# Kernel tuning notes

Measured on AMD Instinct MI355X. Metric: run time of the kernel, lower is better.

Reference implementation:

```python
import jax, jax.numpy as jnp
import numpy as np

N, K, D, H = 16384, 8, 128, 256  # nodes, preds per node, emb dim, hidden


def _build_graph():
    i = np.arange(1, N + 1)[:, None]      # [N,1] node ids 1..N
    k = np.arange(K)[None, :]             # [1,K]
    pred = i - 1 - k                       # predecessor node ids
    mask = pred >= 0
    pred_nodes = np.maximum(pred, 0).astype(np.int32)        # [N,K]
    end = np.repeat(np.arange(1, N + 1), K).astype(np.int32)  # [N*K]
    edges = np.stack([pred_nodes.reshape(-1), end], axis=1)   # [E,2]
    pred_edge_idx = (np.arange(N * K).reshape(N, K) + 1).astype(np.int32)  # +1: zero row prepended to distances
    return pred_nodes, pred_edge_idx, mask, edges.astype(np.int32)


def setup_inputs() -> dict:
    key = jax.random.key(0)
    k1, k2, k3 = jax.random.split(key, 3)
    pred_nodes, pred_edge_idx, mask, edges = _build_graph()
    s1 = 1.0 / np.sqrt(2 * D)
    s2 = 1.0 / np.sqrt(H)
    return {
        "words_embs": jax.random.normal(k1, (N + 1, D), dtype=jnp.float32),
        "W1": jax.random.uniform(k2, (2 * D, H), jnp.float32, -s1, s1),
        "b1": jnp.zeros((H,), jnp.float32),
        "W2": jax.random.uniform(k3, (H, 1), jnp.float32, -s2, s2),
        "b2": jnp.zeros((1,), jnp.float32),
        "best_idxs": jnp.arange(N + 1, dtype=jnp.int32),  # the chain path 0->1->...->N
        "edges": jnp.asarray(edges),
        "pred_nodes": jnp.asarray(pred_nodes),
        "pred_edge_idx": jnp.asarray(pred_edge_idx),
        "pred_mask": jnp.asarray(mask),
    }


def _distance(x, y, W1, b1, W2, b2):
    # MLP over concatenated pair features: Linear -> Tanh -> Linear -> Softplus
    h = jnp.tanh(jnp.concatenate([x, y], axis=-1) @ W1 + b1)
    return jax.nn.softplus(h @ W2 + b2)  # [...,1]


def _forward_alg(words_embs, edges, pred_nodes, pred_edge_idx, pred_mask, W1, b1, W2, b2):
    n_nodes = pred_nodes.shape[0]
    d = _distance(words_embs[edges[:, 0]], words_embs[edges[:, 1]], W1, b1, W2, b2)  # [E,1]
    dists = jnp.concatenate([jnp.zeros((1, 1), d.dtype), d], axis=0)[:, 0]  # [E+1]
    esum0 = jnp.zeros((n_nodes + 1,), d.dtype)
    neg_inf = jnp.asarray(-jnp.inf, d.dtype)

    def step(esum, inp):
        i, preds, eidx, m = inp
        vals = jnp.where(m, esum[preds] - dists[eidx], neg_inf)  # [K]
        mx = jnp.max(vals)
        lse = mx + jnp.log(jnp.sum(jnp.exp(vals - mx)))
        return esum.at[i].set(lse), None

    idxs = jnp.arange(1, n_nodes + 1, dtype=jnp.int32)
    esum, _ = jax.lax.scan(step, esum0, (idxs, pred_nodes, pred_edge_idx, pred_mask))
    return esum[-1]


def reference(words_embs, W1, b1, W2, b2, best_idxs, edges, pred_nodes, pred_edge_idx, pred_mask):
    # gold path score
    feats = words_embs[best_idxs]  # [P,D]
    gold = _distance(feats[:-1], feats[1:], W1, b1, W2, b2).sum(0)  # [1]
    # partition-function-like forward score over the lattice
    fwd = _forward_alg(words_embs, edges, pred_nodes, pred_edge_idx, pred_mask, W1, b1, W2, b2)
    return (gold + fwd).mean()  # single-sample version of loss_fuc
```

## Files before the change

kernel.cpp:

```cpp
#include <hip/hip_runtime.h>
#include <math.h>

#define NNODES 16384
#define NV 16385
#define NEDGE 131072
#define NEG -1e30f
#define SCALE 2.8853900817779268f

typedef __attribute__((ext_vector_type(8))) short short8;
typedef __attribute__((ext_vector_type(8))) unsigned short ushort8;
typedef __attribute__((ext_vector_type(4))) float f32x4;

__device__ float g_part[4 * NEDGE];
__device__ float g_mats[256 * 64];
__device__ float g_mats2[16 * 64];
__device__ float g_gold;

__device__ __forceinline__ unsigned short f2bf(float x) {
  union { float f; unsigned int u; } c; c.f = x;
  unsigned int u = c.u;
  unsigned int r = (u + 0x7fffu + ((u >> 16) & 1u)) >> 16;
  return (unsigned short)r;
}
__device__ __forceinline__ float bf2f(unsigned short u) {
  union { unsigned int u; float f; } c; c.u = ((unsigned int)u) << 16;
  return c.f;
}

__device__ __forceinline__ float lse8(float x0, float x1, float x2, float x3,
                                      float x4, float x5, float x6, float x7) {
  float m = fmaxf(fmaxf(fmaxf(x0, x1), fmaxf(x2, x3)),
                  fmaxf(fmaxf(x4, x5), fmaxf(x6, x7)));
  float s = __expf(x0 - m) + __expf(x1 - m) + __expf(x2 - m) + __expf(x3 - m) +
            __expf(x4 - m) + __expf(x5 - m) + __expf(x6 - m) + __expf(x7 - m);
  return m + __logf(s);
}

__global__ __launch_bounds__(256, 5) void k12_fused(const float* __restrict__ emb,
                                                    const float* __restrict__ W1,
                                                    const float* __restrict__ b1,
                                                    const float* __restrict__ W2) {
  __shared__ unsigned short lds[15072];
  unsigned short* Es  = lds;
  unsigned short* WtA = lds + 5760;
  unsigned short* WtB = lds + 10368;
  unsigned short* CA  = lds;
  unsigned short* CB  = lds + 5760;
  unsigned short* W2s = lds + 14976;
  float* Wsum = (float*)(lds + 15040);

  const int t = threadIdx.x;
  const int h0 = blockIdx.x << 6;
  const int i0 = blockIdx.y << 6;
  if (blockIdx.x == 0 && blockIdx.y == 0 && t == 0) g_gold = 0.f;
  const int wv = t >> 6, lane = t & 63;
  const int l15 = lane & 15, quad = lane >> 4;

  if (t < 64) W2s[t] = f2bf(-2.f * W2[h0 + t]);
  if (t < 8) {
    float s = 0.f;
#pragma unroll
    for (int jj = 0; jj < 8; ++jj) s += W2[h0 + (t << 3) + jj];
    Wsum[t] = s;
  }

  f32x4 accA[5], accB[4];
#pragma unroll
  for (int m = 0; m < 5; ++m) accA[m] = (f32x4){0.f, 0.f, 0.f, 0.f};
#pragma unroll
  for (int m = 0; m < 4; ++m) accB[m] = (f32x4){0.f, 0.f, 0.f, 0.f};

  for (int hk = 0; hk < 2; ++hk) {
    if (hk) __syncthreads();
#pragma unroll
    for (int it = 0; it < 5; ++it) {
      int idx = t + (it << 8);
      int row = idx >> 4;
      int k4 = (idx & 15) << 2;
      int v = i0 - 7 + row;
      float4 g = make_float4(0.f, 0.f, 0.f, 0.f);
      if (v >= 0 && v < NV) g = *(const float4*)&emb[v * 128 + (hk << 6) + k4];
      uint2 pk;
      pk.x = f2bf(g.x) | ((unsigned int)f2bf(g.y) << 16);
      pk.y = f2bf(g.z) | ((unsigned int)f2bf(g.w) << 16);
      *(uint2*)&Es[row * 72 + k4] = pk;
    }
    {
      const int n = t & 63;
      const int kg = (t >> 6) << 4;
#pragma unroll
      for (int kk = 0; kk < 16; kk += 2) {
        int k = (hk << 6) + kg + kk;
        float a0 = W1[k * 256 + h0 + n];
        float a1 = W1[(k + 1) * 256 + h0 + n];
        *(unsigned int*)&WtA[n * 72 + kg + kk] = f2bf(a0) | ((unsigned int)f2bf(a1) << 16);
        float c0 = W1[(128 + k) * 256 + h0 + n];
        float c1 = W1[(128 + k + 1) * 256 + h0 + n];
        *(unsigned int*)&WtB[n * 72 + kg + kk] = f2bf(c0) | ((unsigned int)f2bf(c1) << 16);
      }
    }
    __syncthreads();
    const int kq = quad << 3;
#pragma unroll
    for (int kc = 0; kc < 2; ++kc) {
      const int kb = (kc << 5) + kq;
      short8 fA = *(const short8*)&WtA[((wv << 4) + l15) * 72 + kb];
      short8 fB = *(const short8*)&WtB[((wv << 4) + l15) * 72 + kb];
#pragma unroll
      for (int mf = 0; mf < 5; ++mf) {
        short8 a = *(const short8*)&Es[((mf << 4) + l15) * 72 + kb];
        accA[mf] = __builtin_amdgcn_mfma_f32_16x16x32_bf16(a, fA, accA[mf], 0, 0, 0);
      }
#pragma unroll
      for (int mf = 0; mf < 4; ++mf) {
        short8 a = *(const short8*)&Es[(8 + (mf << 4) + l15) * 72 + kb];
        accB[mf] = __builtin_amdgcn_mfma_f32_16x16x32_bf16(a, fB, accB[mf], 0, 0, 0);
      }
    }
  }
  __syncthreads();
  const int hcol = (wv << 4) + l15;
  const float b1s = b1[h0 + hcol];
#pragma unroll
  for (int mf = 0; mf < 5; ++mf) {
    int rb = (mf << 4) + (quad << 2);
#pragma unroll
    for (int rr = 0; rr < 4; ++rr)
      CA[(rb + rr) * 72 + hcol] = f2bf((accA[mf][rr] + b1s) * SCALE);
  }
#pragma unroll
  for (int mf = 0; mf < 4; ++mf) {
    int rb = (mf << 4) + (quad << 2);
#pragma unroll
    for (int rr = 0; rr < 4; ++rr)
      CB[(rb + rr) * 72 + hcol] = f2bf(accB[mf][rr] * SCALE);
  }
  __syncthreads();
  const int k = t & 7;
  const int qb = t >> 3;
  float part[2] = {0.f, 0.f};
#pragma unroll
  for (int g = 0; g < 8; ++g) {
    const int s = (g + (k << 1)) & 7;
    ushort8 wv8 = *(const ushort8*)&W2s[s << 3];
    float m2w[8];
#pragma unroll
    for (int jj = 0; jj < 8; ++jj) m2w[jj] = bf2f(wv8[jj]);
    const float ws = Wsum[s];
#pragma unroll
    for (int j = 0; j < 2; ++j) {
      const int q = qb + (j << 5);
      ushort8 a8 = *(const ushort8*)&CA[(7 + q - k) * 72 + (s << 3)];
      ushort8 b8 = *(const ushort8*)&CB[q * 72 + (s << 3)];
      float p = part[j];
#pragma unroll
      for (int jj = 0; jj < 8; ++jj) {
        float x = bf2f(a8[jj]) + bf2f(b8[jj]);
        float e = __builtin_amdgcn_exp2f(x);
        float r = __builtin_amdgcn_rcpf(e + 1.f);
        p = fmaf(r, m2w[jj], p);
      }
      part[j] = p + ws;
    }
  }
  const int ebase = blockIdx.x * NEDGE + (blockIdx.y << 9) + t;
  g_part[ebase] = part[0];
  g_part[ebase + 256] = part[1];
}

__global__ __launch_bounds__(256) void k23_chunks(const float* __restrict__ b2) {
  __shared__ float w[64][64];
  __shared__ float red[256];
  const int t = threadIdx.x;
  const int b = blockIdx.x;
  const float b2v = b2[0];
  float gold = 0.f;
#pragma unroll
  for (int it = 0; it < 4; ++it) {
    const int e4 = t + (it << 8);
    const int gidx = (b << 10) + e4;
    float4 s0 = *(const float4*)&g_part[gidx << 2];
    float4 s1 = *(const float4*)&g_part[NEDGE + (gidx << 2)];
    float4 s2 = *(const float4*)&g_part[2 * NEDGE + (gidx << 2)];
    float4 s3 = *(const float4*)&g_part[3 * NEDGE + (gidx << 2)];
    float d0 = s0.x + s1.x + s2.x + s3.x + b2v;
    float d1 = s0.y + s1.y + s2.y + s3.y + b2v;
    float d2 = s0.z + s1.z + s2.z + s3.z + b2v;
    float d3 = s0.w + s1.w + s2.w + s3.w + b2v;
    d0 = fmaxf(d0, 0.f) + log1pf(__expf(-fabsf(d0)));
    d1 = fmaxf(d1, 0.f) + log1pf(__expf(-fabsf(d1)));
    d2 = fmaxf(d2, 0.f) + log1pf(__expf(-fabsf(d2)));
    d3 = fmaxf(d3, 0.f) + log1pf(__expf(-fabsf(d3)));
    const int q = e4 << 2;
    const int cl = q >> 9, r = q & 511;
    const int s = r >> 3, kk = r & 7;
    *(float4*)&w[s][(cl << 3) + kk] = make_float4(d0, d1, d2, d3);
    if ((t & 1) == 0) gold += d0;
  }
  red[t] = gold;
  __syncthreads();
  if (b == 0 && t == 0) {
    for (int s = 0; s < 7; ++s)
      for (int kk = s + 1; kk < 8; ++kk) w[s][kk] = 1e30f;
  }
  for (int o = 128; o > 0; o >>= 1) {
    __syncthreads();
    if (t < o) red[t] += red[t + o];
  }
  __syncthreads();
  if (t == 0) atomicAdd(&g_gold, red[0]);
  if (t < 64) {
    const int g = t >> 3, j = t & 7;
    float P[8];
#pragma unroll
    for (int kk = 0; kk < 8; ++kk) P[kk] = (kk == j) ? 0.f : NEG;
    for (int s = 0; s < 64; ++s) {
      const float* wp = &w[s][g << 3];
      float4 wa = *(const float4*)wp;
      float4 wb = *(const float4*)(wp + 4);
      float nv = lse8(P[0] - wa.x, P[1] - wa.y, P[2] - wa.z, P[3] - wa.w,
                      P[4] - wb.x, P[5] - wb.y, P[6] - wb.z, P[7] - wb.w);
#pragma unroll
      for (int kk = 7; kk > 0; --kk) P[kk] = P[kk - 1];
      P[0] = nv;
    }
    const int c = (b << 3) + g;
    float* mp = &g_mats[(c << 6) + j];
#pragma unroll
    for (int kk = 0; kk < 8; ++kk) mp[kk << 3] = P[kk];
  }
}

__global__ __launch_bounds__(64) void k4_comb() {
  __shared__ float Bm[64];
  const int l = threadIdx.x;
  const int r = blockIdx.x;
  const int i = l >> 3, j = l & 7;
  Bm[l] = g_mats[(r << 10) + l];
  __syncthreads();
  for (int tt = 1; tt < 16; ++tt) {
    const float* __restrict__ A = &g_mats[(((r << 4) + tt) << 6) + (i << 3)];
    float nv = lse8(A[0] + Bm[j], A[1] + Bm[8 + j], A[2] + Bm[16 + j],
                    A[3] + Bm[24 + j], A[4] + Bm[32 + j], A[5] + Bm[40 + j],
                    A[6] + Bm[48 + j], A[7] + Bm[56 + j]);
    __syncthreads();
    Bm[(i << 3) + j] = nv;
    __syncthreads();
  }
  g_mats2[(r << 6) + l] = Bm[l];
}

__global__ __launch_bounds__(64) void k5_final(float* __restrict__ out) {
  __shared__ float Bm[64];
  const int t = threadIdx.x;
  Bm[t] = g_mats2[t];
  __syncthreads();
  const int i = t >> 3, j = t & 7;
  for (int tt = 1; tt < 16; ++tt) {
    const float* __restrict__ A = &g_mats2[(tt << 6) + (i << 3)];
    float nv = lse8(A[0] + Bm[j], A[1] + Bm[8 + j], A[2] + Bm[16 + j],
                    A[3] + Bm[24 + j], A[4] + Bm[32 + j], A[5] + Bm[40 + j],
                    A[6] + Bm[48 + j], A[7] + Bm[56 + j]);
    __syncthreads();
    Bm[(i << 3) + j] = nv;
    __syncthreads();
  }
  if (t == 0) out[0] = g_gold + Bm[0];
}

extern "C" void kernel_launch(void* const* d_in, const int* in_sizes, int n_in,
                              void* d_out, int out_size, void* d_ws, size_t ws_size,
                              hipStream_t stream) {
  const float* emb = (const float*)d_in[0];
  const float* W1 = (const float*)d_in[1];
  const float* b1 = (const float*)d_in[2];
  const float* W2 = (const float*)d_in[3];
  const float* b2 = (const float*)d_in[4];
  float* out = (float*)d_out;
  hipLaunchKernelGGL(k12_fused, dim3(4, 256), dim3(256), 0, stream, emb, W1, b1, W2);
  hipLaunchKernelGGL(k23_chunks, dim3(32), dim3(256), 0, stream, b2);
  hipLaunchKernelGGL(k4_comb, dim3(16), dim3(64), 0, stream);
  hipLaunchKernelGGL(k5_final, dim3(1), dim3(64), 0, stream, out);
}
```

Baseline: 126.5 us.

## Fuse all four kernels into one with last-block-done atomic counters

Merges the MLP edge kernel, the chunk scan, and both log-semiring matrix combine stages into a single launch. The last block to finish each segment, tracked by an atomic ticket, runs the chunk reduction. The last segment then runs the final tree combine using wave shuffles instead of serial LDS loops. This removes three kernel launches and the serial 16-step combine chains, at the cost of threadfence/atomic overhead and tail work serialized on a few blocks. The counters and gold accumulator are reset in-kernel for the next call.

```diff
diff --git a/kernel.cpp b/kernel.cpp
--- a/kernel.cpp
+++ b/kernel.cpp
@@ -12,9 +12,10 @@
 typedef __attribute__((ext_vector_type(4))) float f32x4;
 
 __device__ float g_part[4 * NEDGE];
-__device__ float g_mats[256 * 64];
-__device__ float g_mats2[16 * 64];
+__device__ float g_mats[32 * 64];
 __device__ float g_gold;
+__device__ int g_scnt[32];
+__device__ int g_done;
 
 __device__ __forceinline__ unsigned short f2bf(float x) {
   union { float f; unsigned int u; } c; c.f = x;
@@ -36,11 +37,25 @@
   return m + __logf(s);
 }
 
-__global__ __launch_bounds__(256, 5) void k12_fused(const float* __restrict__ emb,
-                                                    const float* __restrict__ W1,
-                                                    const float* __restrict__ b1,
-                                                    const float* __restrict__ W2) {
-  __shared__ unsigned short lds[15072];
+__device__ __forceinline__ float comb8(float A, float B, int i8, int j) {
+  float x0 = __shfl(A, i8 + 0) + __shfl(B, 0 + j);
+  float x1 = __shfl(A, i8 + 1) + __shfl(B, 8 + j);
+  float x2 = __shfl(A, i8 + 2) + __shfl(B, 16 + j);
+  float x3 = __shfl(A, i8 + 3) + __shfl(B, 24 + j);
+  float x4 = __shfl(A, i8 + 4) + __shfl(B, 32 + j);
+  float x5 = __shfl(A, i8 + 5) + __shfl(B, 40 + j);
+  float x6 = __shfl(A, i8 + 6) + __shfl(B, 48 + j);
+  float x7 = __shfl(A, i8 + 7) + __shfl(B, 56 + j);
+  return lse8(x0, x1, x2, x3, x4, x5, x6, x7);
+}
+
+__global__ __launch_bounds__(256, 5) void k_mega(const float* __restrict__ emb,
+                                                 const float* __restrict__ W1,
+                                                 const float* __restrict__ b1,
+                                                 const float* __restrict__ W2,
+                                                 const float* __restrict__ b2,
+                                                 float* __restrict__ out) {
+  __shared__ __align__(16) unsigned short lds[15072];
   unsigned short* Es  = lds;
   unsigned short* WtA = lds + 5760;
   unsigned short* WtB = lds + 10368;
@@ -48,11 +63,16 @@
   unsigned short* CB  = lds + 5760;
   unsigned short* W2s = lds + 14976;
   float* Wsum = (float*)(lds + 15040);
+  float* wf  = (float*)lds;
+  float* red = (float*)(lds + 8192);
+  float* m8  = (float*)(lds + 8704);
+  float* l2m = (float*)(lds + 9728);
+  __shared__ int s_tick;
 
   const int t = threadIdx.x;
   const int h0 = blockIdx.x << 6;
   const int i0 = blockIdx.y << 6;
-  if (blockIdx.x == 0 && blockIdx.y == 0 && t == 0) g_gold = 0.f;
+  const int seg = blockIdx.y >> 3;
   const int wv = t >> 6, lane = t & 63;
   const int l15 = lane & 15, quad = lane >> 4;
 
@@ -166,13 +186,15 @@
   const int ebase = blockIdx.x * NEDGE + (blockIdx.y << 9) + t;
   g_part[ebase] = part[0];
   g_part[ebase + 256] = part[1];
-}
-
-__global__ __launch_bounds__(256) void k23_chunks(const float* __restrict__ b2) {
-  __shared__ float w[64][64];
-  __shared__ float red[256];
-  const int t = threadIdx.x;
-  const int b = blockIdx.x;
+
+  __threadfence();
+  __syncthreads();
+  if (t == 0) s_tick = atomicAdd(&g_scnt[seg], 1);
+  __syncthreads();
+  if (s_tick != 31) return;
+  __threadfence();
+
+  const int b = seg;
   const float b2v = b2[0];
   float gold = 0.f;
 #pragma unroll
@@ -194,14 +216,14 @@
     const int q = e4 << 2;
     const int cl = q >> 9, r = q & 511;
     const int s = r >> 3, kk = r & 7;
-    *(float4*)&w[s][(cl << 3) + kk] = make_float4(d0, d1, d2, d3);
+    *(float4*)&wf[s * 64 + (cl << 3) + kk] = make_float4(d0, d1, d2, d3);
     if ((t & 1) == 0) gold += d0;
   }
   red[t] = gold;
   __syncthreads();
   if (b == 0 && t == 0) {
     for (int s = 0; s < 7; ++s)
-      for (int kk = s + 1; kk < 8; ++kk) w[s][kk] = 1e30f;
+      for (int kk = s + 1; kk < 8; ++kk) wf[s * 64 + kk] = 1e30f;
   }
   for (int o = 128; o > 0; o >>= 1) {
     __syncthreads();
@@ -215,7 +237,7 @@
 #pragma unroll
     for (int kk = 0; kk < 8; ++kk) P[kk] = (kk == j) ? 0.f : NEG;
     for (int s = 0; s < 64; ++s) {
-      const float* wp = &w[s][g << 3];
+      const float* wp = &wf[s * 64 + (g << 3)];
       float4 wa = *(const float4*)wp;
       float4 wb = *(const float4*)(wp + 4);
       float nv = lse8(P[0] - wa.x, P[1] - wa.y, P[2] - wa.z, P[3] - wa.w,
@@ -224,48 +246,43 @@
       for (int kk = 7; kk > 0; --kk) P[kk] = P[kk - 1];
       P[0] = nv;
     }
-    const int c = (b << 3) + g;
-    float* mp = &g_mats[(c << 6) + j];
-#pragma unroll
-    for (int kk = 0; kk < 8; ++kk) mp[kk << 3] = P[kk];
-  }
-}
-
-__global__ __launch_bounds__(64) void k4_comb() {
-  __shared__ float Bm[64];
-  const int l = threadIdx.x;
-  const int r = blockIdx.x;
-  const int i = l >> 3, j = l & 7;
-  Bm[l] = g_mats[(r << 10) + l];
-  __syncthreads();
-  for (int tt = 1; tt < 16; ++tt) {
-    const float* __restrict__ A = &g_mats[(((r << 4) + tt) << 6) + (i << 3)];
-    float nv = lse8(A[0] + Bm[j], A[1] + Bm[8 + j], A[2] + Bm[16 + j],
-                    A[3] + Bm[24 + j], A[4] + Bm[32 + j], A[5] + Bm[40 + j],
-                    A[6] + Bm[48 + j], A[7] + Bm[56 + j]);
+#pragma unroll
+    for (int kk = 0; kk < 8; ++kk) m8[(g << 6) + (kk << 3) + j] = P[kk];
+    const int i8 = (t >> 3) << 3;
+    float R = m8[t];
+#pragma unroll
+    for (int g2 = 1; g2 < 8; ++g2) R = comb8(m8[(g2 << 6) + t], R, i8, j);
+    g_mats[(b << 6) + t] = R;
+  }
+  __threadfence();
+  __syncthreads();
+  if (t == 0) s_tick = atomicAdd(&g_done, 1);
+  __syncthreads();
+  if (s_tick != 31) return;
+  __threadfence();
+
+  {
+    const int l = t & 63, w = t >> 6;
+    const int i8 = (l >> 3) << 3, j = l & 7;
+    float G = g_mats[((w << 3) << 6) + l];
+#pragma unroll
+    for (int s2 = 1; s2 < 8; ++s2)
+      G = comb8(g_mats[(((w << 3) + s2) << 6) + l], G, i8, j);
+    l2m[(w << 6) + l] = G;
     __syncthreads();
-    Bm[(i << 3) + j] = nv;
-    __syncthreads();
-  }
-  g_mats2[(r << 6) + l] = Bm[l];
-}
-
-__global__ __launch_bounds__(64) void k5_final(float* __restrict__ out) {
-  __shared__ float Bm[64];
-  const int t = threadIdx.x;
-  Bm[t] = g_mats2[t];
-  __syncthreads();
-  const int i = t >> 3, j = t & 7;
-  for (int tt = 1; tt < 16; ++tt) {
-    const float* __restrict__ A = &g_mats2[(tt << 6) + (i << 3)];
-    float nv = lse8(A[0] + Bm[j], A[1] + Bm[8 + j], A[2] + Bm[16 + j],
-                    A[3] + Bm[24 + j], A[4] + Bm[32 + j], A[5] + Bm[40 + j],
-                    A[6] + Bm[48 + j], A[7] + Bm[56 + j]);
-    __syncthreads();
-    Bm[(i << 3) + j] = nv;
-    __syncthreads();
-  }
-  if (t == 0) out[0] = g_gold + Bm[0];
+    if (t < 64) {
+      float G2 = l2m[t];
+#pragma unroll
+      for (int w2 = 1; w2 < 4; ++w2) G2 = comb8(l2m[(w2 << 6) + t], G2, i8, j);
+      if (t == 0) {
+        float gv = atomicAdd(&g_gold, 0.f);
+        out[0] = gv + G2;
+        g_gold = 0.f;
+        g_done = 0;
+      }
+    }
+    if (t < 32) g_scnt[t] = 0;
+  }
 }
 
 extern "C" void kernel_launch(void* const* d_in, const int* in_sizes, int n_in,
@@ -277,8 +294,6 @@
   const float* W2 = (const float*)d_in[3];
   const float* b2 = (const float*)d_in[4];
   float* out = (float*)d_out;
-  hipLaunchKernelGGL(k12_fused, dim3(4, 256), dim3(256), 0, stream, emb, W1, b1, W2);
-  hipLaunchKernelGGL(k23_chunks, dim3(32), dim3(256), 0, stream, b2);
-  hipLaunchKernelGGL(k4_comb, dim3(16), dim3(64), 0, stream);
-  hipLaunchKernelGGL(k5_final, dim3(1), dim3(64), 0, stream, out);
-}
+  hipLaunchKernelGGL(k_mega, dim3(4, 256), dim3(256), 0, stream,
+                     emb, W1, b1, W2, b2, out);
+}
```

Measured after the change: 216.4 us. 71.1% more time.
